# Performance work log

Hardware: AMD Instinct MI355X
Metric: run time of the kernel (lower is better)

## Reference

```python
import jax, jax.numpy as jnp
import numpy as np

C = 256  # input_channels == output_channels (residual add requires it)
EPS = 1e-5


def conv1d(x, w, b):
    # x: [B, Cin, L], w: [Cout, Cin, K], 'same' padding for K=3,p=1
    y = jax.lax.conv_general_dilated(x, w, window_strides=(1,), padding=[(1, 1)],
                                     dimension_numbers=('NCH', 'OIH', 'NCH'))
    return y + b[None, :, None]


def batchnorm(x, gamma, beta):
    # training-mode BN over (batch, length) per channel, biased variance
    m = jnp.mean(x, axis=(0, 2), keepdims=True)
    v = jnp.var(x, axis=(0, 2), keepdims=True)
    return (x - m) * jax.lax.rsqrt(v + EPS) * gamma[None, :, None] + beta[None, :, None]


def cross_attn(q_in, kv_in, res, qw, qb, kw, kb, vw, vb, ow, ob, g, be):
    q = conv1d(q_in, qw, qb)   # [B, C, L]
    k = conv1d(kv_in, kw, kb)  # [B, C, L]
    v = conv1d(kv_in, vw, vb)  # [B, C, L]
    scores = jnp.einsum('bcl,bcm->blm', q, k) / jnp.sqrt(jnp.float32(C))
    probs = jax.nn.softmax(scores, axis=-1)          # [B, L, L]
    ctx = jnp.einsum('blm,bcm->bcl', probs, v)       # [B, C, L]
    return batchnorm(conv1d(ctx, ow, ob), g, be) + res


def setup_inputs() -> dict:
    key = jax.random.key(0)
    ks = jax.random.split(key, 24)
    B, L = 16, 1024
    d = {
        'image': jax.random.normal(ks[0], (B, C, L), jnp.float32),
        'clinical': jax.random.normal(ks[1], (B, 1, L), jnp.float32),
    }
    def w(k, shape):
        return jax.random.normal(k, shape, jnp.float32) * 0.05
    # branch a: cli_to_img (query from image, key/value from clinical)
    d['a_qw'] = w(ks[2], (C, C, 3)); d['a_qb'] = w(ks[3], (C,))
    d['a_kw'] = w(ks[4], (C, 1, 3)); d['a_kb'] = w(ks[5], (C,))
    d['a_vw'] = w(ks[6], (C, 1, 3)); d['a_vb'] = w(ks[7], (C,))
    d['a_ow'] = w(ks[8], (C, C, 3)); d['a_ob'] = w(ks[9], (C,))
    d['a_g'] = jnp.ones((C,), jnp.float32); d['a_beta'] = jnp.zeros((C,), jnp.float32)
    # branch b: img_to_cli (query from clinical, key/value from image)
    d['b_qw'] = w(ks[10], (C, 1, 3)); d['b_qb'] = w(ks[11], (C,))
    d['b_kw'] = w(ks[12], (C, C, 3)); d['b_kb'] = w(ks[13], (C,))
    d['b_vw'] = w(ks[14], (C, C, 3)); d['b_vb'] = w(ks[15], (C,))
    d['b_ow'] = w(ks[16], (C, C, 3)); d['b_ob'] = w(ks[17], (C,))
    d['b_g'] = jnp.ones((C,), jnp.float32); d['b_beta'] = jnp.zeros((C,), jnp.float32)
    return d


def reference(image, clinical,
              a_qw, a_qb, a_kw, a_kb, a_vw, a_vb, a_ow, a_ob, a_g, a_beta,
              b_qw, b_qb, b_kw, b_kb, b_vw, b_vb, b_ow, b_ob, b_g, b_beta):
    cli_to_img = cross_attn(image, clinical, image,
                            a_qw, a_qb, a_kw, a_kb, a_vw, a_vb, a_ow, a_ob, a_g, a_beta)
    img_to_cli = cross_attn(clinical, image, image,
                            b_qw, b_qb, b_kw, b_kb, b_vw, b_vb, b_ow, b_ob, b_g, b_beta)
    return jnp.concatenate([cli_to_img, img_to_cli], axis=1)  # [B, 2C, L]
```

## Files before the change

kernel.cpp:

```cpp
#include <hip/hip_runtime.h>


typedef short bf16x8 __attribute__((ext_vector_type(8)));
typedef float f32x4 __attribute__((ext_vector_type(4)));

__device__ __forceinline__ unsigned short f2bf(float f) {
    union { float f; unsigned u; } v; v.f = f;
    unsigned r = v.u + 0x7fffu + ((v.u >> 16) & 1u);
    return (unsigned short)(r >> 16);
}
__device__ __forceinline__ float bf2f(unsigned short h) {
    union { unsigned u; float f; } v; v.u = ((unsigned)h) << 16;
    return v.f;
}

__device__ __forceinline__ void glds16(const void* g, void* l) {
    __builtin_amdgcn_global_load_lds(
        (const __attribute__((address_space(1))) unsigned int*)g,
        (__attribute__((address_space(3))) unsigned int*)l, 16, 0, 0);
}

#define TM 128
#define TN 128
#define BK 32

struct GOp {
    const unsigned short* A; const unsigned short* B; void* C;
    long sA, sB, sC;
    int lda, ldb, ldc, nxt, nyt, nz, K;
    const float* bias_row; const float* bias_col;
    const float* row_scale;
    float* stats; int stat_base;
};

__global__ __launch_bounds__(256)
void gemm_nt(GOp op0, GOp op1, int n0, float alpha)
{
    __shared__ __attribute__((aligned(16))) char sh[34816];
    unsigned short* shs = (unsigned short*)sh;
    int id = blockIdx.x;
    const bool brn = (id >= n0);
    const GOp op = brn ? op1 : op0;
    if (brn) id -= n0;
    const int bz = id % op.nz;
    const int rem = id / op.nz;
    const int by = rem / op.nxt;
    const int bx = rem - by * op.nxt;

    const unsigned short* Ab = op.A + op.sA * bz;
    const unsigned short* Bb = op.B + op.sB * bz;
    const int lda = op.lda, ldb = op.ldb;
    const int i0 = by * TM;
    const int j0 = bx * TN;
    const int t = threadIdx.x;
    const int lane = t & 63;
    const int wave = t >> 6;
    const int wm = wave & 1, wn = wave >> 1;

    const int srow = wave * 16 + (lane >> 2);
    const int sc8 = (lane & 3) * 8;
    const unsigned short* gA0 = Ab + (long)(i0 + srow) * lda + sc8;
    const unsigned short* gA1 = gA0 + (long)64 * lda;
    const unsigned short* gB0 = Bb + (long)(j0 + srow) * ldb + sc8;
    const unsigned short* gB1 = gB0 + (long)64 * ldb;
    const int d0 = wave * 512;
    const int d1 = 2048 + wave * 512;

    f32x4 acc[4][4];
#pragma unroll
    for (int a_ = 0; a_ < 4; ++a_)
#pragma unroll
        for (int b_ = 0; b_ < 4; ++b_)
            acc[a_][b_] = (f32x4){0.f, 0.f, 0.f, 0.f};

    const int frow = lane & 15;
    const int fk = (lane >> 4) * 8;

    glds16(gA0, shs + d0);
    glds16(gA1, shs + d1);
    glds16(gB0, shs + 8192 + d0);
    glds16(gB1, shs + 8192 + d1);

    int cur = 0;
    for (int k0 = 0; k0 < op.K; k0 += BK) {
        __syncthreads();
        const int kn = k0 + BK;
        if (kn < op.K) {
            const int nb = cur ^ 1;
            glds16(gA0 + kn, shs + nb * 4096 + d0);
            glds16(gA1 + kn, shs + nb * 4096 + d1);
            glds16(gB0 + kn, shs + 8192 + nb * 4096 + d0);
            glds16(gB1 + kn, shs + 8192 + nb * 4096 + d1);
        }
        const unsigned short* la = shs + cur * 4096;
        const unsigned short* lb = shs + 8192 + cur * 4096;
        bf16x8 af[4], bfr[4];
#pragma unroll
        for (int mt = 0; mt < 4; ++mt)
            af[mt] = *(const bf16x8*)(&la[(wm * 64 + mt * 16 + frow) * BK + fk]);
#pragma unroll
        for (int nt = 0; nt < 4; ++nt)
            bfr[nt] = *(const bf16x8*)(&lb[(wn * 64 + nt * 16 + frow) * BK + fk]);
#pragma unroll
        for (int mt = 0; mt < 4; ++mt)
#pragma unroll
            for (int nt = 0; nt < 4; ++nt)
                acc[mt][nt] = __builtin_amdgcn_mfma_f32_16x16x32_bf16(af[mt], bfr[nt], acc[mt][nt], 0, 0, 0);
        cur ^= 1;
    }

    const int lr = (lane >> 4) * 4;
    const int lc = lane & 15;
    __syncthreads();

    unsigned short* tile = shs;
#pragma unroll
    for (int mt = 0; mt < 4; ++mt) {
#pragma unroll
        for (int nt = 0; nt < 4; ++nt) {
            const int col = wn * 64 + nt * 16 + lc;
            const float bc = op.bias_col ? op.bias_col[j0 + col] : 0.f;
#pragma unroll
            for (int r = 0; r < 4; ++r) {
                const int row = wm * 64 + mt * 16 + lr + r;
                const float brv = op.bias_row ? op.bias_row[i0 + row] : 0.f;
                const float rsv = op.row_scale
                    ? op.row_scale[(long)bz * (op.nyt * TM) + i0 + row] : 1.f;
                tile[row * 136 + col] = f2bf((acc[mt][nt][r] * alpha + brv + bc) * rsv);
            }
        }
    }
    __syncthreads();
    unsigned short* Cb = (unsigned short*)op.C + op.sC * bz;
#pragma unroll
    for (int p = 0; p < 8; ++p) {
        const int cid = p * 256 + t;
        const int row = cid >> 4;
        const int c8 = (cid & 15) * 8;
        const uint4 v = *(const uint4*)(tile + row * 136 + c8);
        *(uint4*)(Cb + (long)(i0 + row) * op.ldc + j0 + c8) = v;
    }
    if (op.stats) {
        const int row = t >> 1, half = t & 1;
        float s = 0.f, s2 = 0.f;
#pragma unroll
        for (int c = 0; c < 64; c += 8) {
            const bf16x8 v = *(const bf16x8*)(tile + row * 136 + half * 64 + c);
#pragma unroll
            for (int e = 0; e < 8; ++e) {
                const float f = bf2f((unsigned short)v[e]);
                s += f; s2 += f * f;
            }
        }
        s += __shfl_xor(s, 1);
        s2 += __shfl_xor(s2, 1);
        if (half == 0) {
            const int ch = op.stat_base + i0 + row;
            atomicAdd(&op.stats[ch], s);
            atomicAdd(&op.stats[512 + ch], s2);
        }
    }
}

__global__ __launch_bounds__(256)
void mats(const unsigned short* __restrict__ QK,
          const float* __restrict__ a_kw, const float* __restrict__ a_kb,
          const float* __restrict__ b_qw, const float* __restrict__ b_qb,
          float* __restrict__ M4A, float* __restrict__ M4Y)
{
    const int z = blockIdx.x >> 2;
    const int l = ((blockIdx.x & 3) << 8) + threadIdx.x;
    const unsigned short* row = QK + ((long)z * 1024 + l) * 512;
    float a0 = 0.f, a1 = 0.f, a2 = 0.f, d = 0.f;
    float y0 = 0.f, y1 = 0.f, y2 = 0.f, cb = 0.f;
    for (int c8 = 0; c8 < 32; ++c8) {
        const bf16x8 q = *(const bf16x8*)(row + c8 * 8);
        const bf16x8 k = *(const bf16x8*)(row + 256 + c8 * 8);
#pragma unroll
        for (int e = 0; e < 8; ++e) {
            const int c = c8 * 8 + e;
            const float qv = bf2f((unsigned short)q[e]);
            const float kv = bf2f((unsigned short)k[e]);
            a0 += qv * a_kw[c * 3];     a1 += qv * a_kw[c * 3 + 1];
            a2 += qv * a_kw[c * 3 + 2]; d  += qv * a_kb[c];
            y0 += kv * b_qw[c * 3];     y1 += kv * b_qw[c * 3 + 1];
            y2 += kv * b_qw[c * 3 + 2]; cb += kv * b_qb[c];
        }
    }
    const long o = ((long)z * 1024 + l) * 4;
    *(float4*)(M4A + o) = make_float4(a0, a1, a2, d);
    *(float4*)(M4Y + o) = make_float4(y0, y1, y2, cb);
}

__global__ __launch_bounds__(256)
void attn_mid(const float* __restrict__ cli,
              const float* __restrict__ M4A, const float* __restrict__ M4Y,
              const float* __restrict__ a_vw, const float* __restrict__ a_vb,
              unsigned short* __restrict__ P, float* __restrict__ invl,
              unsigned short* __restrict__ ctxT)
{
    __shared__ __attribute__((aligned(16))) float smem[1032 + 256];
    const int bid = blockIdx.x;
    const int t = threadIdx.x;
    if (bid < 256) {
        const int z = bid & 15;
        const int l0 = (bid >> 4) << 6;
        float* xs = smem;
        float* tt = smem + 1032;
        for (int i = t; i < 1026; i += 256) {
            const int l = i - 1;
            xs[i] = (l >= 0 && l < 1024) ? cli[(long)z * 1024 + l] : 0.f;
        }
        __syncthreads();
        const int r = t >> 2, q = t & 3;
        const float4 A = *(const float4*)(M4A + ((long)z * 1024 + l0 + r) * 4);
        float t0 = 0.f, t1 = 0.f, t2 = 0.f, ls = 0.f;
        const int m0 = q * 256;
#pragma unroll 4
        for (int m = m0; m < m0 + 256; ++m) {
            const float x0 = xs[m], x1 = xs[m + 1], x2 = xs[m + 2];
            const float e = __expf((A.x * x0 + A.y * x1 + A.z * x2 + A.w) * 0.0625f);
            t0 += e * x0; t1 += e * x1; t2 += e * x2; ls += e;
        }
        t0 += __shfl_xor(t0, 1); t0 += __shfl_xor(t0, 2);
        t1 += __shfl_xor(t1, 1); t1 += __shfl_xor(t1, 2);
        t2 += __shfl_xor(t2, 1); t2 += __shfl_xor(t2, 2);
        ls += __shfl_xor(ls, 1); ls += __shfl_xor(ls, 2);
        if (q == 0) *(float4*)(tt + r * 4) = make_float4(t0, t1, t2, ls);
        __syncthreads();
        const float wv0 = a_vw[t * 3], wv1 = a_vw[t * 3 + 1], wv2 = a_vw[t * 3 + 2];
        const float bv = a_vb[t];
        unsigned short* Ob = ctxT + ((long)z * 1026 + 1 + l0) * 256;
        for (int rr = 0; rr < 64; ++rr) {
            const float4 th = *(const float4*)(tt + rr * 4);
            const float inv = 1.f / th.w;
            Ob[(long)rr * 256 + t] = f2bf((wv0 * th.x + wv1 * th.y + wv2 * th.z) * inv + bv);
        }
    } else {
        const int b2 = bid - 256;
        const int z = b2 & 15;
        const int l0 = (b2 >> 4) << 4;
        const int li = t >> 4, mg = t & 15;
        const int l = l0 + li;
        const float x0 = (l >= 1) ? cli[(long)z * 1024 + l - 1] : 0.f;
        const float x1 = cli[(long)z * 1024 + l];
        const float x2 = (l < 1023) ? cli[(long)z * 1024 + l + 1] : 0.f;
        const float4* Yz = (const float4*)(M4Y + (long)z * 4096);
        unsigned short* Pr = P + ((long)z * 1024 + l) * 1024;
        float lsum = 0.f;
#pragma unroll
        for (int jc = 0; jc < 4; ++jc)
#pragma unroll
            for (int i8 = 0; i8 < 2; ++i8) {
                const int mb = jc * 256 + mg * 16 + i8 * 8;
                bf16x8 out;
#pragma unroll
                for (int e = 0; e < 8; ++e) {
                    const float4 y = Yz[mb + e];
                    const float p = __expf((x0 * y.x + x1 * y.y + x2 * y.z + y.w) * 0.0625f);
                    lsum += p;
                    out[e] = (short)f2bf(p);
                }
                *(bf16x8*)(Pr + mb) = out;
            }
        lsum += __shfl_xor(lsum, 1); lsum += __shfl_xor(lsum, 2);
        lsum += __shfl_xor(lsum, 4); lsum += __shfl_xor(lsum, 8);
        if (mg == 0) invl[(long)z * 1024 + l] = 1.f / lsum;
    }
}

__global__ __launch_bounds__(256)
void prep(const float* __restrict__ image,
          const float* __restrict__ a_qw, const float* __restrict__ a_qb,
          const float* __restrict__ b_kw, const float* __restrict__ b_kb,
          const float* __restrict__ b_vw,
          const float* __restrict__ a_ow, const float* __restrict__ b_ow,
          unsigned short* __restrict__ imgT, unsigned short* __restrict__ ctxT,
          unsigned short* __restrict__ W, float* __restrict__ qkb,
          float* __restrict__ sums)
{
    __shared__ char smem[64 * 65 * 4];
    const int b = blockIdx.x;
    const int t = threadIdx.x;
    if (b < 1024) {
        float* tile = (float*)smem;
        const int bt = b >> 6, rem = b & 63;
        const int l0 = (rem & 15) * 64, c0 = (rem >> 4) * 64;
        const float* xb = image + ((long)bt * 256 + c0) * 1024 + l0;
        for (int idx = t; idx < 4096; idx += 256) {
            const int cc = idx >> 6, ll = idx & 63;
            tile[cc * 65 + ll] = xb[(long)cc * 1024 + ll];
        }
        __syncthreads();
        unsigned short* op = imgT + ((long)bt * 1026 + l0 + 1) * 256 + c0;
        for (int idx = t; idx < 4096; idx += 256) {
            const int ll = idx >> 6, cc = idx & 63;
            op[(long)ll * 256 + cc] = f2bf(tile[cc * 65 + ll]);
        }
    } else if (b < 4864) {
        const int i = (b - 1024) * 256 + t;
        const int row = i / 768;
        const int kk = i - row * 768;
        const int j = kk >> 8, ci = kk & 255;
        const float* src = (row < 256) ? a_qw : (row < 512) ? b_kw
                         : (row < 768) ? b_vw : (row < 1024) ? a_ow : b_ow;
        const int r = row & 255;
        W[i] = f2bf(src[r * 768 + ci * 3 + j]);
    } else {
        const int i = (b - 4864) * 256 + t;
        if (i < 512) {
            qkb[i] = (i < 256) ? a_qb[i] : b_kb[i - 256];
        } else if (i < 512 + 8192) {
            const int p = i - 512;
            const int bi = p >> 9, rr = (p >> 8) & 1, c = p & 255;
            imgT[((long)bi * 1026 + (rr ? 1025 : 0)) * 256 + c] = 0;
        } else if (i < 512 + 8192 + 16384) {
            const int p = i - 512 - 8192;
            const int bz = p >> 9, rr = (p >> 8) & 1, c = p & 255;
            ctxT[((long)bz * 1026 + (rr ? 1025 : 0)) * 256 + c] = 0;
        } else if (i < 512 + 8192 + 16384 + 1024) {
            sums[i - 512 - 8192 - 16384] = 0.f;
        }
    }
}

__global__ __launch_bounds__(256)
void bn_finalize(const float* __restrict__ sums,
                 const float* __restrict__ ag, const float* __restrict__ abeta,
                 const float* __restrict__ bg, const float* __restrict__ bbeta,
                 float* __restrict__ ss)
{
    const int ch = blockIdx.x * 256 + threadIdx.x;
    const int branch = ch >> 8, c = ch & 255;
    const float mean = sums[ch] * (1.f / 16384.f);
    const float var = sums[512 + ch] * (1.f / 16384.f) - mean * mean;
    const float inv = rsqrtf(var + 1e-5f);
    const float g = branch ? bg[c] : ag[c];
    const float be = branch ? bbeta[c] : abeta[c];
    const float sc = g * inv;
    ss[ch] = sc;
    ss[512 + ch] = be - mean * sc;
}

__global__ __launch_bounds__(256)
void bn_apply(const unsigned short* __restrict__ Y, const float* __restrict__ img,
              const float* __restrict__ ss, float* __restrict__ out)
{
    const long i4 = (long)blockIdx.x * 256 + threadIdx.x;
    const long e = i4 * 4;
    const int l = (int)(e & 1023);
    const int ch = (int)((e >> 10) & 511);
    const int b = (int)(e >> 19);
    const int branch = ch >> 8, c = ch & 255;
    const float sc = ss[ch], sh = ss[512 + ch];
    const long yoff = (((long)(branch * 16 + b)) * 256 + c) * 1024 + l;
    const long ioff = ((long)b * 256 + c) * 1024 + l;
    const ushort4 yv = *(const ushort4*)(Y + yoff);
    const float4 iv = *(const float4*)(img + ioff);
    float4 o;
    o.x = bf2f(yv.x) * sc + sh + iv.x;
    o.y = bf2f(yv.y) * sc + sh + iv.y;
    o.z = bf2f(yv.z) * sc + sh + iv.z;
    o.w = bf2f(yv.w) * sc + sh + iv.w;
    *(float4*)(out + e) = o;
}

extern "C" void kernel_launch(void* const* d_in, const int* in_sizes, int n_in,
                              void* d_out, int out_size, void* d_ws, size_t ws_size,
                              hipStream_t stream)
{
    const float* image    = (const float*)d_in[0];
    const float* clinical = (const float*)d_in[1];
    const float* a_qw = (const float*)d_in[2];  const float* a_qb = (const float*)d_in[3];
    const float* a_kw = (const float*)d_in[4];  const float* a_kb = (const float*)d_in[5];
    const float* a_vw = (const float*)d_in[6];  const float* a_vb = (const float*)d_in[7];
    const float* a_ow = (const float*)d_in[8];  const float* a_ob = (const float*)d_in[9];
    const float* a_g  = (const float*)d_in[10]; const float* a_be = (const float*)d_in[11];
    const float* b_qw = (const float*)d_in[12]; const float* b_qb = (const float*)d_in[13];
    const float* b_kw = (const float*)d_in[14]; const float* b_kb = (const float*)d_in[15];
    const float* b_vw = (const float*)d_in[16]; const float* b_vb = (const float*)d_in[17];
    const float* b_ow = (const float*)d_in[18]; const float* b_ob = (const float*)d_in[19];
    const float* b_g  = (const float*)d_in[20]; const float* b_be = (const float*)d_in[21];
    float* out = (float*)d_out;

    char* ws = (char*)d_ws;
    const long MB = 1048576L;
    unsigned short* imgT = (unsigned short*)(ws);
    unsigned short* ctxT = (unsigned short*)(ws + 9 * MB);
    unsigned short* vb   = (unsigned short*)(ws + 54 * MB);
    unsigned short* QK   = (unsigned short*)(ws + 62 * MB);
    unsigned short* P    = (unsigned short*)(ws + 80 * MB);
    float*          M4A  = (float*)(ws + 114 * MB);
    float*          M4Y  = (float*)(ws + 115 * MB);
    float*          invl = (float*)(ws + 116 * MB);
    unsigned short* Y    = (unsigned short*)(ws + 142 * MB);
    unsigned short* W    = (unsigned short*)(ws + 174 * MB);
    float*          qkb  = (float*)(ws + 176 * MB);
    float*          ss   = qkb + 512;
    float*          sums = qkb + 1536;
    unsigned short* Wqk = W;
    unsigned short* Wvb = W + 512L * 768;
    unsigned short* Woa = W + 768L * 768;
    unsigned short* Wob = W + 1024L * 768;

    const dim3 blk(256);
    const long sIT = 1026L * 256, sQK = 1024L * 512, sV = 256L * 1024;
    const long sP = 1024L * 1024;

    prep<<<4966, blk, 0, stream>>>(image, a_qw, a_qb, b_kw, b_kb, b_vw,
                                   a_ow, b_ow, imgT, ctxT, W, qkb, sums);
    {
        GOp opQ = {imgT, Wqk, QK, sIT, 0, sQK, 256, 768, 512, 4, 8, 16, 768,
                   nullptr, qkb, nullptr, nullptr, 0};
        GOp opV = {Wvb, imgT, vb, 0, sIT, sV, 768, 256, 1024, 8, 2, 16, 768,
                   b_vb, nullptr, nullptr, nullptr, 0};
        gemm_nt<<<768, blk, 0, stream>>>(opQ, opV, 512, 1.f);
    }
    mats<<<64, blk, 0, stream>>>(QK, a_kw, a_kb, b_qw, b_qb, M4A, M4Y);
    attn_mid<<<1280, blk, 0, stream>>>(clinical, M4A, M4Y, a_vw, a_vb,
                                       P, invl, ctxT);
    {
        GOp opA = {Woa, ctxT, Y, 0, sIT, sV, 768, 256, 1024, 8, 2, 16, 768,
                   a_ob, nullptr, nullptr, sums, 0};
        GOp opPV = {P, vb, ctxT + 16 * sIT + 256, sP, sV, sIT, 1024, 1024, 256,
                    2, 8, 16, 1024, nullptr, nullptr, invl, nullptr, 0};
        gemm_nt<<<512, blk, 0, stream>>>(opA, opPV, 256, 1.f);
    }
    {
        GOp opB = {Wob, ctxT + 16 * sIT, Y + 16 * sV, 0, sIT, sV, 768, 256, 1024,
                   8, 2, 16, 768, b_ob, nullptr, nullptr, sums, 256};
        gemm_nt<<<256, blk, 0, stream>>>(opB, opB, 256, 1.f);
    }
    bn_finalize<<<2, blk, 0, stream>>>(sums, a_g, a_be, b_g, b_be, ss);
    bn_apply<<<8192, blk, 0, stream>>>(Y, image, ss, out);
}
```

Measured before the change: 266.5 us.

## Fold rank-1 query/key projections into precomputed weight products, drop QK GEMM

```diff
diff --git a/kernel.cpp b/kernel.cpp
--- a/kernel.cpp
+++ b/kernel.cpp
@@ -163,33 +163,46 @@
 }
 
 __global__ __launch_bounds__(256)
-void mats(const unsigned short* __restrict__ QK,
-          const float* __restrict__ a_kw, const float* __restrict__ a_kb,
-          const float* __restrict__ b_qw, const float* __restrict__ b_qb,
-          float* __restrict__ M4A, float* __restrict__ M4Y)
-{
-    const int z = blockIdx.x >> 2;
-    const int l = ((blockIdx.x & 3) << 8) + threadIdx.x;
-    const unsigned short* row = QK + ((long)z * 1024 + l) * 512;
-    float a0 = 0.f, a1 = 0.f, a2 = 0.f, d = 0.f;
-    float y0 = 0.f, y1 = 0.f, y2 = 0.f, cb = 0.f;
-    for (int c8 = 0; c8 < 32; ++c8) {
-        const bf16x8 q = *(const bf16x8*)(row + c8 * 8);
-        const bf16x8 k = *(const bf16x8*)(row + 256 + c8 * 8);
+void matsAY(const unsigned short* __restrict__ imgT,
+            const float* __restrict__ EF, const float* __restrict__ cst,
+            float* __restrict__ M4A, float* __restrict__ M4Y)
+{
+    const int bid = blockIdx.x;
+    const int z = bid & 15, chk = bid >> 4;
+    const int t = threadIdx.x;
+    const int r = t >> 2, q = t & 3;
+    const int l = chk * 64 + r;
+    const unsigned short* w = imgT + ((long)z * 1026 + l) * 256 + q * 192;
+    const float* ef = EF + q * 192 * 8;
+    float a0 = 0.f, a1 = 0.f, a2 = 0.f, a3 = 0.f;
+    float y0 = 0.f, y1 = 0.f, y2 = 0.f, y3 = 0.f;
+#pragma unroll 4
+    for (int kk = 0; kk < 192; kk += 8) {
+        const bf16x8 x8 = *(const bf16x8*)(w + kk);
 #pragma unroll
         for (int e = 0; e < 8; ++e) {
-            const int c = c8 * 8 + e;
-            const float qv = bf2f((unsigned short)q[e]);
-            const float kv = bf2f((unsigned short)k[e]);
-            a0 += qv * a_kw[c * 3];     a1 += qv * a_kw[c * 3 + 1];
-            a2 += qv * a_kw[c * 3 + 2]; d  += qv * a_kb[c];
-            y0 += kv * b_qw[c * 3];     y1 += kv * b_qw[c * 3 + 1];
-            y2 += kv * b_qw[c * 3 + 2]; cb += kv * b_qb[c];
-        }
-    }
-    const long o = ((long)z * 1024 + l) * 4;
-    *(float4*)(M4A + o) = make_float4(a0, a1, a2, d);
-    *(float4*)(M4Y + o) = make_float4(y0, y1, y2, cb);
+            const float xf = bf2f((unsigned short)x8[e]);
+            const float4 E = *(const float4*)(ef + (kk + e) * 8);
+            const float4 F = *(const float4*)(ef + (kk + e) * 8 + 4);
+            a0 += xf * E.x; a1 += xf * E.y; a2 += xf * E.z; a3 += xf * E.w;
+            y0 += xf * F.x; y1 += xf * F.y; y2 += xf * F.z; y3 += xf * F.w;
+        }
+    }
+    a0 += __shfl_xor(a0, 1); a0 += __shfl_xor(a0, 2);
+    a1 += __shfl_xor(a1, 1); a1 += __shfl_xor(a1, 2);
+    a2 += __shfl_xor(a2, 1); a2 += __shfl_xor(a2, 2);
+    a3 += __shfl_xor(a3, 1); a3 += __shfl_xor(a3, 2);
+    y0 += __shfl_xor(y0, 1); y0 += __shfl_xor(y0, 2);
+    y1 += __shfl_xor(y1, 1); y1 += __shfl_xor(y1, 2);
+    y2 += __shfl_xor(y2, 1); y2 += __shfl_xor(y2, 2);
+    y3 += __shfl_xor(y3, 1); y3 += __shfl_xor(y3, 2);
+    if (q == 0) {
+        const float4 e0 = *(const float4*)cst;
+        const float4 f0 = *(const float4*)(cst + 4);
+        const long o = ((long)z * 1024 + l) * 4;
+        *(float4*)(M4A + o) = make_float4(a0 + e0.x, a1 + e0.y, a2 + e0.z, a3 + e0.w);
+        *(float4*)(M4Y + o) = make_float4(y0 + f0.x, y1 + f0.y, y2 + f0.z, y3 + f0.w);
+    }
 }
 
 __global__ __launch_bounds__(256)
@@ -219,7 +232,7 @@
 #pragma unroll 4
         for (int m = m0; m < m0 + 256; ++m) {
             const float x0 = xs[m], x1 = xs[m + 1], x2 = xs[m + 2];
-            const float e = __expf((A.x * x0 + A.y * x1 + A.z * x2 + A.w) * 0.0625f);
+            const float e = __expf(A.x * x0 + A.y * x1 + A.z * x2 + A.w);
             t0 += e * x0; t1 += e * x1; t2 += e * x2; ls += e;
         }
         t0 += __shfl_xor(t0, 1); t0 += __shfl_xor(t0, 2);
@@ -257,7 +270,7 @@
 #pragma unroll
                 for (int e = 0; e < 8; ++e) {
                     const float4 y = Yz[mb + e];
-                    const float p = __expf((x0 * y.x + x1 * y.y + x2 * y.z + y.w) * 0.0625f);
+                    const float p = __expf(x0 * y.x + x1 * y.y + x2 * y.z + y.w);
                     lsum += p;
                     out[e] = (short)f2bf(p);
                 }
@@ -272,11 +285,14 @@
 __global__ __launch_bounds__(256)
 void prep(const float* __restrict__ image,
           const float* __restrict__ a_qw, const float* __restrict__ a_qb,
+          const float* __restrict__ a_kw, const float* __restrict__ a_kb,
+          const float* __restrict__ b_qw, const float* __restrict__ b_qb,
           const float* __restrict__ b_kw, const float* __restrict__ b_kb,
           const float* __restrict__ b_vw,
           const float* __restrict__ a_ow, const float* __restrict__ b_ow,
           unsigned short* __restrict__ imgT, unsigned short* __restrict__ ctxT,
-          unsigned short* __restrict__ W, float* __restrict__ qkb,
+          unsigned short* __restrict__ W,
+          float* __restrict__ EF, float* __restrict__ cst,
           float* __restrict__ sums)
 {
     __shared__ char smem[64 * 65 * 4];
@@ -297,29 +313,53 @@
             const int ll = idx >> 6, cc = idx & 63;
             op[(long)ll * 256 + cc] = f2bf(tile[cc * 65 + ll]);
         }
-    } else if (b < 4864) {
+    } else if (b < 3328) {
         const int i = (b - 1024) * 256 + t;
         const int row = i / 768;
         const int kk = i - row * 768;
         const int j = kk >> 8, ci = kk & 255;
-        const float* src = (row < 256) ? a_qw : (row < 512) ? b_kw
-                         : (row < 768) ? b_vw : (row < 1024) ? a_ow : b_ow;
+        const float* src = (row < 256) ? b_vw : (row < 512) ? a_ow : b_ow;
         const int r = row & 255;
         W[i] = f2bf(src[r * 768 + ci * 3 + j]);
-    } else {
-        const int i = (b - 4864) * 256 + t;
-        if (i < 512) {
-            qkb[i] = (i < 256) ? a_qb[i] : b_kb[i - 256];
-        } else if (i < 512 + 8192) {
-            const int p = i - 512;
-            const int bi = p >> 9, rr = (p >> 8) & 1, c = p & 255;
+    } else if (b < 3428) {
+        const int i = (b - 3328) * 256 + t;
+        if (i < 8192) {
+            const int bi = i >> 9, rr = (i >> 8) & 1, c = i & 255;
             imgT[((long)bi * 1026 + (rr ? 1025 : 0)) * 256 + c] = 0;
-        } else if (i < 512 + 8192 + 16384) {
-            const int p = i - 512 - 8192;
+        } else if (i < 8192 + 16384) {
+            const int p = i - 8192;
             const int bz = p >> 9, rr = (p >> 8) & 1, c = p & 255;
             ctxT[((long)bz * 1026 + (rr ? 1025 : 0)) * 256 + c] = 0;
-        } else if (i < 512 + 8192 + 16384 + 1024) {
-            sums[i - 512 - 8192 - 16384] = 0.f;
+        } else {
+            sums[i - 8192 - 16384] = 0.f;
+        }
+    } else if (b < 3431) {
+        const int k = (b - 3428) * 256 + t;
+        const int ci = k & 255, j = k >> 8;
+        float e0 = 0.f, e1 = 0.f, e2 = 0.f, e3 = 0.f;
+        float f0 = 0.f, f1 = 0.f, f2 = 0.f, f3 = 0.f;
+        for (int c = 0; c < 256; ++c) {
+            const float qa = a_qw[c * 768 + ci * 3 + j];
+            e0 += qa * a_kw[c * 3];     e1 += qa * a_kw[c * 3 + 1];
+            e2 += qa * a_kw[c * 3 + 2]; e3 += qa * a_kb[c];
+            const float kb = b_kw[c * 768 + ci * 3 + j];
+            f0 += kb * b_qw[c * 3];     f1 += kb * b_qw[c * 3 + 1];
+            f2 += kb * b_qw[c * 3 + 2]; f3 += kb * b_qb[c];
+        }
+        float* o = EF + (long)k * 8;
+        o[0] = e0 * 0.0625f; o[1] = e1 * 0.0625f; o[2] = e2 * 0.0625f; o[3] = e3 * 0.0625f;
+        o[4] = f0 * 0.0625f; o[5] = f1 * 0.0625f; o[6] = f2 * 0.0625f; o[7] = f3 * 0.0625f;
+    } else {
+        if (t < 8) {
+            float s = 0.f;
+            if (t < 4) {
+                for (int c = 0; c < 256; ++c)
+                    s += a_qb[c] * ((t < 3) ? a_kw[c * 3 + t] : a_kb[c]);
+            } else {
+                for (int c = 0; c < 256; ++c)
+                    s += b_kb[c] * ((t < 7) ? b_qw[c * 3 + (t - 4)] : b_qb[c]);
+            }
+            cst[t] = s * 0.0625f;
         }
     }
 }
@@ -388,37 +428,35 @@
     unsigned short* imgT = (unsigned short*)(ws);
     unsigned short* ctxT = (unsigned short*)(ws + 9 * MB);
     unsigned short* vb   = (unsigned short*)(ws + 54 * MB);
-    unsigned short* QK   = (unsigned short*)(ws + 62 * MB);
     unsigned short* P    = (unsigned short*)(ws + 80 * MB);
     float*          M4A  = (float*)(ws + 114 * MB);
     float*          M4Y  = (float*)(ws + 115 * MB);
     float*          invl = (float*)(ws + 116 * MB);
     unsigned short* Y    = (unsigned short*)(ws + 142 * MB);
     unsigned short* W    = (unsigned short*)(ws + 174 * MB);
-    float*          qkb  = (float*)(ws + 176 * MB);
-    float*          ss   = qkb + 512;
-    float*          sums = qkb + 1536;
-    unsigned short* Wqk = W;
-    unsigned short* Wvb = W + 512L * 768;
-    unsigned short* Woa = W + 768L * 768;
-    unsigned short* Wob = W + 1024L * 768;
+    float*          EF   = (float*)(ws + 176 * MB);
+    float*          cst  = EF + 6144;
+    float*          ss   = EF + 6208;
+    float*          sums = EF + 7232;
+    unsigned short* Wvb = W;
+    unsigned short* Woa = W + 256L * 768;
+    unsigned short* Wob = W + 512L * 768;
 
     const dim3 blk(256);
-    const long sIT = 1026L * 256, sQK = 1024L * 512, sV = 256L * 1024;
+    const long sIT = 1026L * 256, sV = 256L * 1024;
     const long sP = 1024L * 1024;
 
-    prep<<<4966, blk, 0, stream>>>(image, a_qw, a_qb, b_kw, b_kb, b_vw,
-                                   a_ow, b_ow, imgT, ctxT, W, qkb, sums);
+    prep<<<3432, blk, 0, stream>>>(image, a_qw, a_qb, a_kw, a_kb,
+                                   b_qw, b_qb, b_kw, b_kb, b_vw, a_ow, b_ow,
+                                   imgT, ctxT, W, EF, cst, sums);
+    matsAY<<<256, blk, 0, stream>>>(imgT, EF, cst, M4A, M4Y);
+    attn_mid<<<1280, blk, 0, stream>>>(clinical, M4A, M4Y, a_vw, a_vb,
+                                       P, invl, ctxT);
     {
-        GOp opQ = {imgT, Wqk, QK, sIT, 0, sQK, 256, 768, 512, 4, 8, 16, 768,
-                   nullptr, qkb, nullptr, nullptr, 0};
         GOp opV = {Wvb, imgT, vb, 0, sIT, sV, 768, 256, 1024, 8, 2, 16, 768,
                    b_vb, nullptr, nullptr, nullptr, 0};
-        gemm_nt<<<768, blk, 0, stream>>>(opQ, opV, 512, 1.f);
-    }
-    mats<<<64, blk, 0, stream>>>(QK, a_kw, a_kb, b_qw, b_qb, M4A, M4Y);
-    attn_mid<<<1280, blk, 0, stream>>>(clinical, M4A, M4Y, a_vw, a_vb,
-                                       P, invl, ctxT);
+        gemm_nt<<<256, blk, 0, stream>>>(opV, opV, 256, 1.f);
+    }
     {
         GOp opA = {Woa, ctxT, Y, 0, sIT, sV, 768, 256, 1024, 8, 2, 16, 768,
                    a_ob, nullptr, nullptr, sums, 0};
```

New measurement: 313.3 us. 1.18x slower.
